# Optimization experiments

Hardware: AMD Instinct MI355X
Metric: run time of the kernel (lower is better)

The kernel has to match this reference:

```python
import math
import jax, jax.numpy as jnp
import numpy as np

DIM = 1024
N_HEADS = 16
HEAD_DIM = DIM // N_HEADS
SEQ_LEN = 2048
BASE = 10000.0
EPS = 1e-5


def rope_cache(seq_len, dim):
    pos = jnp.arange(seq_len, dtype=jnp.float32)[:, None]          # (S,1)
    di = jnp.arange(0, dim, 2, dtype=jnp.float32) / dim            # (d/2,)
    theta = pos * jnp.exp(-di * math.log(BASE))                    # (S,d/2)
    cos = jnp.repeat(jnp.cos(theta), 2, axis=1)                    # (S,d)
    sin = jnp.repeat(jnp.sin(theta), 2, axis=1)
    return cos, sin


def rotate_half(x):
    # NOTE: faithful to source: concatenate (-odd, even), not interleave
    x1 = x[..., ::2]
    x2 = x[..., 1::2]
    return jnp.concatenate((-x2, x1), axis=-1)


def layernorm(x, gamma, beta):
    mu = jnp.mean(x, axis=-1, keepdims=True)
    var = jnp.var(x, axis=-1, keepdims=True)
    return (x - mu) * jax.lax.rsqrt(var + EPS) * gamma + beta


def setup_inputs() -> dict:
    key = jax.random.key(0)
    ks = jax.random.split(key, 7)
    s = 1.0 / math.sqrt(DIM)
    return {
        "x": jax.random.normal(ks[0], (2, SEQ_LEN, DIM), dtype=jnp.float32),
        "Wq": jax.random.normal(ks[1], (DIM, DIM), dtype=jnp.float32) * s,
        "Wk": jax.random.normal(ks[2], (DIM, DIM), dtype=jnp.float32) * s,
        "Wv": jax.random.normal(ks[3], (DIM, DIM), dtype=jnp.float32) * s,
        "q_gamma": jnp.ones((HEAD_DIM,), jnp.float32),
        "q_beta": jnp.zeros((HEAD_DIM,), jnp.float32),
        "k_gamma": jnp.ones((HEAD_DIM,), jnp.float32),
        "k_beta": jnp.zeros((HEAD_DIM,), jnp.float32),
        "Wo": jax.random.normal(ks[4], (DIM, DIM), dtype=jnp.float32) * s,
        "bo": jnp.zeros((DIM,), jnp.float32),
    }


def reference(x, Wq, Wk, Wv, q_gamma, q_beta, k_gamma, k_beta, Wo, bo):
    B, S, D = x.shape
    H, hd = N_HEADS, HEAD_DIM
    # QKV projections (torch Linear: x @ W.T)
    q = (x @ Wq.T).reshape(B, S, H, hd).transpose(0, 2, 1, 3)  # (B,H,S,hd)
    k = (x @ Wk.T).reshape(B, S, H, hd).transpose(0, 2, 1, 3)
    v = (x @ Wv.T).reshape(B, S, H, hd).transpose(0, 2, 1, 3)
    # QK-norm over head_dim
    q = layernorm(q, q_gamma, q_beta)
    k = layernorm(k, k_gamma, k_beta)
    # RoPE
    cos, sin = rope_cache(S, hd)  # (S,hd)
    cos = cos[None, None]
    sin = sin[None, None]
    q = q * cos + rotate_half(q) * sin
    k = k * cos + rotate_half(k) * sin
    # causal attention
    scale = 1.0 / math.sqrt(hd)
    scores = scale * jnp.einsum('bhqd,bhkd->bhqk', q, k)
    mask = jnp.tril(jnp.ones((S, S), dtype=bool))
    scores = jnp.where(mask, scores, -jnp.inf)
    attn = jax.nn.softmax(scores, axis=-1)
    out = jnp.einsum('bhqk,bhkd->bhqd', attn, v)
    out = out.transpose(0, 2, 1, 3).reshape(B, S, D)
    return out @ Wo.T + bo
```

## Files before the change

### kernel.cpp

```cpp
#include <hip/hip_runtime.h>
#include <hip/hip_bf16.h>

#define SEQ   2048
#define NH    16
#define HD    64
#define BATCH 2
#define DIMM  1024

typedef __attribute__((ext_vector_type(8))) __bf16 bfrag;
typedef __attribute__((ext_vector_type(4))) float f32x4;

__device__ __forceinline__ short f2b(float f) {
  unsigned x = __float_as_uint(f);
  x += 0x7fff + ((x >> 16) & 1);
  return (short)(x >> 16);
}
__device__ __forceinline__ float b2f(short s) {
  unsigned u = ((unsigned)(unsigned short)s) << 16;
  return __uint_as_float(u);
}
__device__ __forceinline__ short f2b_pk(float f) {
  unsigned r;
  asm("v_cvt_pk_bf16_f32 %0, %1, %1" : "=v"(r) : "v"(f));
  return (short)r;
}

__device__ __forceinline__ void gload16(const void* g, void* l) {
  __builtin_amdgcn_global_load_lds(
      (const __attribute__((address_space(1))) void*)g,
      (__attribute__((address_space(3))) void*)l, 16, 0, 0);
}

__global__ __launch_bounds__(256) void k_prep(
    const float* __restrict__ x, const float* __restrict__ w0,
    const float* __restrict__ w1, const float* __restrict__ w2,
    const float* __restrict__ w3, short* __restrict__ xb,
    short* __restrict__ wb, float* __restrict__ cstab) {
  int b = blockIdx.x;
  if (b < 4096) {
    int i = b * 256 + threadIdx.x;
    float4 v = reinterpret_cast<const float4*>(x)[i];
    short4 o;
    o.x = f2b(v.x); o.y = f2b(v.y); o.z = f2b(v.z); o.w = f2b(v.w);
    reinterpret_cast<short4*>(xb)[i] = o;
  } else if (b < 8192) {
    int bb = b - 4096;
    int widx = bb >> 10;
    const float* src = widx == 0 ? w0 : (widx == 1 ? w1 : (widx == 2 ? w2 : w3));
    int i = (bb & 1023) * 256 + threadIdx.x;
    float4 v = reinterpret_cast<const float4*>(src)[i];
    short4 o;
    o.x = f2b(v.x); o.y = f2b(v.y); o.z = f2b(v.z); o.w = f2b(v.w);
    reinterpret_cast<short4*>(wb + (size_t)widx * 1048576)[i] = o;
  } else {
    int gid = (b - 8192) * 256 + threadIdx.x;
    int s = gid >> 5, i = gid & 31;
    float freq = expf(-(float)(2 * i) * (1.0f / 64.0f) * 9.210340371976184f);
    float th = (float)s * freq;
    cstab[gid * 2]     = cosf(th);
    cstab[gid * 2 + 1] = sinf(th);
  }
}

__global__ __launch_bounds__(256) void k_gemm_qkv(
    const short* __restrict__ xb, const short* __restrict__ wb,
    short* __restrict__ Qh, short* __restrict__ Kh, short* __restrict__ Vt) {
  __shared__ alignas(16) short As[2][128 * 64];
  __shared__ alignas(16) short Bs[2][128 * 64];
  const int tid = threadIdx.x;
  const int lane = tid & 63, w = tid >> 6;
  const int wr = w >> 1, wc = w & 1;
  const int id = blockIdx.x;
  const int xcd = id & 7, j = id >> 3;
  const int bn = xcd * 3 + j % 3;
  const int bm = j / 3;
  const int widx = bn >> 3;
  const int brow0 = (bn & 7) * 128;
  const short* Wp = wb + (size_t)widx * (1 << 20);

  const int l15 = lane & 15, lq = lane >> 4, l7 = lane & 7;
  const int srow = lane >> 3;
  const int sslot = l7 ^ srow;

  f32x4 acc[4][4] = {};

  auto STAGE = [&](int buf, int kk) {
#pragma unroll
    for (int p = 0; p < 4; ++p) {
      int rr = p * 32 + w * 8 + srow;
      gload16(&xb[(size_t)(bm * 128 + rr) * 1024 + kk + sslot * 8],
              &As[buf][p * 2048 + w * 512]);
      gload16(&Wp[(size_t)(brow0 + rr) * 1024 + kk + sslot * 8],
              &Bs[buf][p * 2048 + w * 512]);
    }
  };

  STAGE(0, 0);
  __syncthreads();
  int cur = 0;
#pragma unroll 1
  for (int t = 0; t < 16; ++t) {
    if (t + 1 < 16) STAGE(cur ^ 1, (t + 1) * 64);
#pragma unroll
    for (int ks = 0; ks < 2; ++ks) {
      bfrag af[4], bf[4];
      int slot = (ks * 4 + lq) ^ l7;
#pragma unroll
      for (int mi = 0; mi < 4; ++mi)
        af[mi] = *(const bfrag*)&As[cur][(wr * 64 + mi * 16 + l15) * 64 + slot * 8];
#pragma unroll
      for (int ni = 0; ni < 4; ++ni)
        bf[ni] = *(const bfrag*)&Bs[cur][(wc * 64 + ni * 16 + l15) * 64 + slot * 8];
      __builtin_amdgcn_s_setprio(1);
#pragma unroll
      for (int mi = 0; mi < 4; ++mi)
#pragma unroll
        for (int ni = 0; ni < 4; ++ni)
          acc[mi][ni] = __builtin_amdgcn_mfma_f32_16x16x32_bf16(af[mi], bf[ni], acc[mi][ni], 0, 0, 0);
      __builtin_amdgcn_s_setprio(0);
    }
    __syncthreads();
    cur ^= 1;
  }

  if (widx < 2) {
    short* dst = widx == 0 ? Qh : Kh;
#pragma unroll
    for (int mi = 0; mi < 4; ++mi) {
#pragma unroll
      for (int ni = 0; ni < 4; ++ni) {
        int ng = bn * 128 + wc * 64 + ni * 16 + l15;
        int col = ng & 1023, h = col >> 6, d = col & 63;
#pragma unroll
        for (int r = 0; r < 4; ++r) {
          int mg = bm * 128 + wr * 64 + mi * 16 + lq * 4 + r;
          int b = mg >> 11, s = mg & 2047;
          dst[((size_t)((b * 16 + h) * 2048 + s)) * 64 + d] = f2b(acc[mi][ni][r]);
        }
      }
    }
  } else {
#pragma unroll
    for (int mi = 0; mi < 4; ++mi) {
#pragma unroll
      for (int ni = 0; ni < 4; ++ni) {
        int ng = bn * 128 + wc * 64 + ni * 16 + l15;
        int col = ng & 1023, h = col >> 6, d = col & 63;
        int mg0 = bm * 128 + wr * 64 + mi * 16 + lq * 4;
        int b = mg0 >> 11, s0 = mg0 & 2047;
        short4 sv;
        sv.x = f2b(acc[mi][ni][0]); sv.y = f2b(acc[mi][ni][1]);
        sv.z = f2b(acc[mi][ni][2]); sv.w = f2b(acc[mi][ni][3]);
        *reinterpret_cast<short4*>(
            &Vt[((size_t)((b * 16 + h) * 64 + d)) * 2048 + s0]) = sv;
      }
    }
  }
}

__global__ __launch_bounds__(256) void k_ln_rope(
    short* __restrict__ Qh, short* __restrict__ Kh,
    const float* __restrict__ qg, const float* __restrict__ qb_,
    const float* __restrict__ kg, const float* __restrict__ kb_,
    const float* __restrict__ cstab) {
  __shared__ float Ysh[32 * 64];
  const int tid = threadIdx.x;
  const int rloc = tid >> 3;
  const int g = tid & 7;
  const int d0 = g * 8;
  const int row = blockIdx.x * 32 + rloc;
  const int which = blockIdx.y;
  short* ptr = which ? Kh : Qh;
  const float* gamma = which ? kg : qg;
  const float* beta  = which ? kb_ : qb_;
  const int s = row & 2047;

  short vs[8];
  *reinterpret_cast<uint4*>(vs) =
      *reinterpret_cast<const uint4*>(&ptr[(size_t)row * 64 + d0]);
  float x[8];
#pragma unroll
  for (int j = 0; j < 8; ++j) x[j] = b2f(vs[j]);
  float s1 = 0.0f, s2 = 0.0f;
#pragma unroll
  for (int j = 0; j < 8; ++j) { s1 += x[j]; s2 = fmaf(x[j], x[j], s2); }
#pragma unroll
  for (int off = 1; off < 8; off <<= 1) {
    s1 += __shfl_xor(s1, off, 8);
    s2 += __shfl_xor(s2, off, 8);
  }
  float mu = s1 * (1.0f / 64.0f);
  float var = s2 * (1.0f / 64.0f) - mu * mu;
  float rs = rsqrtf(var + 1e-5f);

  float gv[8], bv[8];
  *reinterpret_cast<float4*>(&gv[0]) = *reinterpret_cast<const float4*>(&gamma[d0]);
  *reinterpret_cast<float4*>(&gv[4]) = *reinterpret_cast<const float4*>(&gamma[d0 + 4]);
  *reinterpret_cast<float4*>(&bv[0]) = *reinterpret_cast<const float4*>(&beta[d0]);
  *reinterpret_cast<float4*>(&bv[4]) = *reinterpret_cast<const float4*>(&beta[d0 + 4]);
  float y[8];
#pragma unroll
  for (int j = 0; j < 8; ++j) y[j] = (x[j] - mu) * rs * gv[j] + bv[j];

  *reinterpret_cast<float4*>(&Ysh[rloc * 64 + d0])     = *reinterpret_cast<float4*>(&y[0]);
  *reinterpret_cast<float4*>(&Ysh[rloc * 64 + d0 + 4]) = *reinterpret_cast<float4*>(&y[4]);
  __syncthreads();

  float2 cs4[4];
  *reinterpret_cast<float4*>(&cs4[0]) =
      *reinterpret_cast<const float4*>(&cstab[((size_t)s * 32 + g * 4) * 2]);
  *reinterpret_cast<float4*>(&cs4[2]) =
      *reinterpret_cast<const float4*>(&cstab[((size_t)s * 32 + g * 4 + 2) * 2]);

  short o[8];
#pragma unroll
  for (int j = 0; j < 8; ++j) {
    int d = d0 + j;
    float pv = (d < 32) ? Ysh[rloc * 64 + 2 * d + 1]
                        : Ysh[rloc * 64 + 2 * (d - 32)];
    float c = cs4[j >> 1].x, sn = cs4[j >> 1].y;
    float ov = (d < 32) ? (y[j] * c - pv * sn) : (y[j] * c + pv * sn);
    o[j] = f2b_pk(ov);
  }
  *reinterpret_cast<uint4*>(&ptr[(size_t)row * 64 + d0]) =
      *reinterpret_cast<uint4*>(o);
}

__global__ __launch_bounds__(256) void k_attn(
    const short* __restrict__ Qh, const short* __restrict__ Kh,
    const short* __restrict__ Vtg, short* __restrict__ Ob) {
  __shared__ alignas(16) short Ks[2][64 * 64];
  __shared__ alignas(16) short Vs[2][64 * 64];
  __shared__ alignas(16) short Ps[4][16 * 64];
  const int id = blockIdx.x;
  const int xcd = id & 7;
  const int idx = id >> 3;
  const int qt = 31 - (idx >> 2);
  const int bh = xcd * 4 + (idx & 3);
  const int b = bh >> 4, h = bh & 15;
  const int tid = threadIdx.x, lane = tid & 63, w = tid >> 6;
  const short* Qp = Qh + (size_t)bh * SEQ * 64;
  const short* Kp = Kh + (size_t)bh * SEQ * 64;
  const short* Vp = Vtg + (size_t)bh * 64 * SEQ;

  const int srow = lane >> 3;
  const int sslot = (lane & 7) ^ srow;

  const int l15 = lane & 15;
  const int l7 = lane & 7;
  const int lq = lane >> 4;

  auto STAGE = [&](int buf, int kb) {
#pragma unroll
    for (int j = 0; j < 2; ++j) {
      int rr = w * 16 + j * 8 + srow;
      gload16(&Kp[(size_t)(kb * 64 + rr) * 64 + sslot * 8],
              &Ks[buf][w * 1024 + j * 512]);
      gload16(&Vp[(size_t)rr * 2048 + kb * 64 + sslot * 8],
              &Vs[buf][w * 1024 + j * 512]);
    }
  };

  const int nkb = qt + 1;

  const int qrow_l = qt * 64 + w * 16 + l15;
  bfrag qf[2];
#pragma unroll
  for (int c = 0; c < 2; ++c)
    qf[c] = *(const bfrag*)&Qp[(size_t)qrow_l * 64 + c * 32 + lq * 8];

  f32x4 oacc[4] = {};
  float lrow[4] = {0.0f, 0.0f, 0.0f, 0.0f};

  auto body = [&](int kb, int cur, bool diag) {
    f32x4 sacc[4] = {};
    __builtin_amdgcn_s_setprio(1);
#pragma unroll
    for (int c2 = 0; c2 < 4; ++c2) {
      int krow = c2 * 16 + l15;
#pragma unroll
      for (int dc = 0; dc < 2; ++dc) {
        int slot = (dc * 4 + lq) ^ l7;
        bfrag kf = *(const bfrag*)&Ks[cur][krow * 64 + slot * 8];
        sacc[c2] = __builtin_amdgcn_mfma_f32_16x16x32_bf16(qf[dc], kf, sacc[c2], 0, 0, 0);
      }
    }
    __builtin_amdgcn_s_setprio(0);

    const int qg0 = qt * 64 + w * 16 + lq * 4;
#pragma unroll
    for (int r = 0; r < 4; ++r) {
      float pv4[4];
#pragma unroll
      for (int c2 = 0; c2 < 4; ++c2) {
        float s2 = fmaf(sacc[c2][r], 0.18033688011112042f, -11.541560327111707f);
        if (diag && (kb * 64 + c2 * 16 + l15 > qg0 + r)) s2 = -1e30f;
        pv4[c2] = __builtin_amdgcn_exp2f(s2);
      }
      lrow[r] += (pv4[0] + pv4[1]) + (pv4[2] + pv4[3]);
      int row = lq * 4 + r;
#pragma unroll
      for (int c2 = 0; c2 < 4; ++c2) {
        int swz = (c2 * 2 + (l15 >> 3)) ^ (row & 7);
        Ps[w][row * 64 + swz * 8 + (l15 & 7)] = f2b_pk(pv4[c2]);
      }
    }

    bfrag pf[2];
#pragma unroll
    for (int kf2 = 0; kf2 < 2; ++kf2)
      pf[kf2] = *(const bfrag*)&Ps[w][l15 * 64 + (((kf2 * 4 + lq) ^ l7) * 8)];
    __builtin_amdgcn_s_setprio(1);
#pragma unroll
    for (int dc = 0; dc < 4; ++dc) {
      int drow = dc * 16 + l15;
#pragma unroll
      for (int kf2 = 0; kf2 < 2; ++kf2) {
        int slot = (kf2 * 4 + lq) ^ l7;
        bfrag vf = *(const bfrag*)&Vs[cur][drow * 64 + slot * 8];
        oacc[dc] = __builtin_amdgcn_mfma_f32_16x16x32_bf16(pf[kf2], vf, oacc[dc], 0, 0, 0);
      }
    }
    __builtin_amdgcn_s_setprio(0);
  };

  STAGE(0, 0);
  __syncthreads();

  int cur = 0;
#pragma unroll 1
  for (int kb = 0; kb < nkb - 1; ++kb) {
    STAGE(cur ^ 1, kb + 1);
    body(kb, cur, false);
    __syncthreads();
    cur ^= 1;
  }
  body(nkb - 1, cur, true);

  float inv[4];
#pragma unroll
  for (int r = 0; r < 4; ++r) {
#pragma unroll
    for (int off = 1; off < 16; off <<= 1) lrow[r] += __shfl_xor(lrow[r], off);
    inv[r] = 1.0f / lrow[r];
  }
#pragma unroll
  for (int dc = 0; dc < 4; ++dc) {
#pragma unroll
    for (int r = 0; r < 4; ++r) {
      int qg = qt * 64 + w * 16 + lq * 4 + r;
      Ob[(size_t)(b * SEQ + qg) * 1024 + h * 64 + dc * 16 + l15] =
          f2b(oacc[dc][r] * inv[r]);
    }
  }
}

__global__ __launch_bounds__(256) void k_gemm_out(
    const short* __restrict__ Ab, const short* __restrict__ Wp,
    const float* __restrict__ bo, float* __restrict__ out) {
  __shared__ alignas(16) short As[2][64 * 64];
  __shared__ alignas(16) short Bs[2][128 * 64];
  const int tid = threadIdx.x;
  const int lane = tid & 63, w = tid >> 6;
  const int id = blockIdx.x;
  const int bn = id & 7, bm = id >> 3;
  const int brow0 = bn * 128;

  const int l15 = lane & 15, lq = lane >> 4, l7 = lane & 7;
  const int srow = lane >> 3;
  const int sslot = l7 ^ srow;

  f32x4 acc[4][2] = {};

  auto STAGE = [&](int buf, int kk) {
#pragma unroll
    for (int p = 0; p < 2; ++p) {
      int rr = p * 32 + w * 8 + srow;
      gload16(&Ab[(size_t)(bm * 64 + rr) * 1024 + kk + sslot * 8],
              &As[buf][p * 2048 + w * 512]);
    }
#pragma unroll
    for (int p = 0; p < 4; ++p) {
      int rr = p * 32 + w * 8 + srow;
      gload16(&Wp[(size_t)(brow0 + rr) * 1024 + kk + sslot * 8],
              &Bs[buf][p * 2048 + w * 512]);
    }
  };

  STAGE(0, 0);
  __syncthreads();
  int cur = 0;
#pragma unroll 1
  for (int t = 0; t < 16; ++t) {
    if (t + 1 < 16) STAGE(cur ^ 1, (t + 1) * 64);
#pragma unroll
    for (int ks = 0; ks < 2; ++ks) {
      bfrag af[4], bf[2];
      int slot = (ks * 4 + lq) ^ l7;
#pragma unroll
      for (int mi = 0; mi < 4; ++mi)
        af[mi] = *(const bfrag*)&As[cur][(mi * 16 + l15) * 64 + slot * 8];
#pragma unroll
      for (int ni = 0; ni < 2; ++ni)
        bf[ni] = *(const bfrag*)&Bs[cur][(w * 32 + ni * 16 + l15) * 64 + slot * 8];
      __builtin_amdgcn_s_setprio(1);
#pragma unroll
      for (int mi = 0; mi < 4; ++mi)
#pragma unroll
        for (int ni = 0; ni < 2; ++ni)
          acc[mi][ni] = __builtin_amdgcn_mfma_f32_16x16x32_bf16(af[mi], bf[ni], acc[mi][ni], 0, 0, 0);
      __builtin_amdgcn_s_setprio(0);
    }
    __syncthreads();
    cur ^= 1;
  }

#pragma unroll
  for (int mi = 0; mi < 4; ++mi) {
#pragma unroll
    for (int ni = 0; ni < 2; ++ni) {
      int ng = bn * 128 + w * 32 + ni * 16 + l15;
      float bias = bo[ng];
#pragma unroll
      for (int r = 0; r < 4; ++r) {
        int mg = bm * 64 + mi * 16 + lq * 4 + r;
        out[(size_t)mg * 1024 + ng] = acc[mi][ni][r] + bias;
      }
    }
  }
}

extern "C" void kernel_launch(void* const* d_in, const int* in_sizes, int n_in,
                              void* d_out, int out_size, void* d_ws, size_t ws_size,
                              hipStream_t stream) {
  const float* x  = (const float*)d_in[0];
  const float* Wq = (const float*)d_in[1];
  const float* Wk = (const float*)d_in[2];
  const float* Wv = (const float*)d_in[3];
  const float* qgamma = (const float*)d_in[4];
  const float* qbeta  = (const float*)d_in[5];
  const float* kgamma = (const float*)d_in[6];
  const float* kbeta  = (const float*)d_in[7];
  const float* Wo = (const float*)d_in[8];
  const float* bo = (const float*)d_in[9];
  float* out = (float*)d_out;

  char* ws = (char*)d_ws;
  short* xb    = (short*)(ws);
  short* wb    = (short*)(ws + 8388608);
  short* Qh    = (short*)(ws + 16777216);
  short* Kh    = (short*)(ws + 25165824);
  short* Vt    = (short*)(ws + 33554432);
  short* Obuf  = (short*)(ws + 41943040);
  float* cstab = (float*)(ws + 50331648);

  k_prep<<<8448, 256, 0, stream>>>(x, Wq, Wk, Wv, Wo, xb, wb, cstab);

  k_gemm_qkv<<<768, 256, 0, stream>>>(xb, wb, Qh, Kh, Vt);
  k_ln_rope<<<dim3(2048, 2), 256, 0, stream>>>(
      Qh, Kh, qgamma, qbeta, kgamma, kbeta, cstab);
  k_attn<<<1024, 256, 0, stream>>>(Qh, Kh, Vt, Obuf);
  k_gemm_out<<<512, 256, 0, stream>>>(Obuf, wb + 3145728, bo, out);
}
```

Measured before the change: 117.8 us.

## Transpose QK^T MFMA to pass P to PV via register shuffles, drop LDS staging

Swaps the MFMA operand order for the score computation so each lane holds scores for one query row across four keys. The probabilities are then packed to bf16 pairs and redistributed with cross-lane shuffles into the A-fragment layout for the PV MFMA, which removes the per-wave shared-memory P buffer and its write/read round trip. Row sums become a single accumulator reduced across lane groups at the end. In exchange it adds 16 shuffles (ds_bpermute) plus selects per block, which may cost about as much as the LDS traffic it replaces.

After: 120.6 us. 1.02x slower.

```diff
diff --git a/kernel.cpp b/kernel.cpp
--- a/kernel.cpp
+++ b/kernel.cpp
@@ -23,6 +23,11 @@
   unsigned r;
   asm("v_cvt_pk_bf16_f32 %0, %1, %1" : "=v"(r) : "v"(f));
   return (short)r;
+}
+__device__ __forceinline__ unsigned cvtpk2(float lo, float hi) {
+  unsigned r;
+  asm("v_cvt_pk_bf16_f32 %0, %1, %2" : "=v"(r) : "v"(lo), "v"(hi));
+  return r;
 }
 
 __device__ __forceinline__ void gload16(const void* g, void* l) {
@@ -231,7 +236,6 @@
     const short* __restrict__ Vtg, short* __restrict__ Ob) {
   __shared__ alignas(16) short Ks[2][64 * 64];
   __shared__ alignas(16) short Vs[2][64 * 64];
-  __shared__ alignas(16) short Ps[4][16 * 64];
   const int id = blockIdx.x;
   const int xcd = id & 7;
   const int idx = id >> 3;
@@ -270,7 +274,11 @@
     qf[c] = *(const bfrag*)&Qp[(size_t)qrow_l * 64 + c * 32 + lq * 8];
 
   f32x4 oacc[4] = {};
-  float lrow[4] = {0.0f, 0.0f, 0.0f, 0.0f};
+  float lrow = 0.0f;
+
+  const int src_a = l15 + (((2 * lq) & 3) << 4);
+  const int src_b = l15 + (((2 * lq + 1) & 3) << 4);
+  const bool hisel = (lq >> 1) != 0;
 
   auto body = [&](int kb, int cur, bool diag) {
     f32x4 sacc[4] = {};
@@ -282,34 +290,50 @@
       for (int dc = 0; dc < 2; ++dc) {
         int slot = (dc * 4 + lq) ^ l7;
         bfrag kf = *(const bfrag*)&Ks[cur][krow * 64 + slot * 8];
-        sacc[c2] = __builtin_amdgcn_mfma_f32_16x16x32_bf16(qf[dc], kf, sacc[c2], 0, 0, 0);
+        sacc[c2] = __builtin_amdgcn_mfma_f32_16x16x32_bf16(kf, qf[dc], sacc[c2], 0, 0, 0);
       }
     }
     __builtin_amdgcn_s_setprio(0);
 
-    const int qg0 = qt * 64 + w * 16 + lq * 4;
-#pragma unroll
-    for (int r = 0; r < 4; ++r) {
-      float pv4[4];
-#pragma unroll
-      for (int c2 = 0; c2 < 4; ++c2) {
+    const int qg = qt * 64 + w * 16 + l15;
+    float p[4][4];
+#pragma unroll
+    for (int c2 = 0; c2 < 4; ++c2) {
+      int k0 = kb * 64 + c2 * 16 + lq * 4;
+#pragma unroll
+      for (int r = 0; r < 4; ++r) {
         float s2 = fmaf(sacc[c2][r], 0.18033688011112042f, -11.541560327111707f);
-        if (diag && (kb * 64 + c2 * 16 + l15 > qg0 + r)) s2 = -1e30f;
-        pv4[c2] = __builtin_amdgcn_exp2f(s2);
-      }
-      lrow[r] += (pv4[0] + pv4[1]) + (pv4[2] + pv4[3]);
-      int row = lq * 4 + r;
-#pragma unroll
-      for (int c2 = 0; c2 < 4; ++c2) {
-        int swz = (c2 * 2 + (l15 >> 3)) ^ (row & 7);
-        Ps[w][row * 64 + swz * 8 + (l15 & 7)] = f2b_pk(pv4[c2]);
-      }
-    }
-
+        if (diag && (k0 + r > qg)) s2 = -1e30f;
+        p[c2][r] = __builtin_amdgcn_exp2f(s2);
+      }
+      lrow += (p[c2][0] + p[c2][1]) + (p[c2][2] + p[c2][3]);
+    }
+
+    unsigned pk[4][2];
+#pragma unroll
+    for (int c2 = 0; c2 < 4; ++c2) {
+      pk[c2][0] = cvtpk2(p[c2][0], p[c2][1]);
+      pk[c2][1] = cvtpk2(p[c2][2], p[c2][3]);
+    }
     bfrag pf[2];
 #pragma unroll
-    for (int kf2 = 0; kf2 < 2; ++kf2)
-      pf[kf2] = *(const bfrag*)&Ps[w][l15 * 64 + (((kf2 * 4 + lq) ^ l7) * 8)];
+    for (int kf2 = 0; kf2 < 2; ++kf2) {
+      unsigned u[4];
+#pragma unroll
+      for (int bhalf = 0; bhalf < 2; ++bhalf) {
+        int src = bhalf ? src_b : src_a;
+        unsigned lo0 = __shfl(pk[2 * kf2][0], src);
+        unsigned lo1 = __shfl(pk[2 * kf2][1], src);
+        unsigned hi0 = __shfl(pk[2 * kf2 + 1][0], src);
+        unsigned hi1 = __shfl(pk[2 * kf2 + 1][1], src);
+        u[bhalf * 2 + 0] = hisel ? hi0 : lo0;
+        u[bhalf * 2 + 1] = hisel ? hi1 : lo1;
+      }
+      union { bfrag f; unsigned v[4]; } uu;
+      uu.v[0] = u[0]; uu.v[1] = u[1]; uu.v[2] = u[2]; uu.v[3] = u[3];
+      pf[kf2] = uu.f;
+    }
+
     __builtin_amdgcn_s_setprio(1);
 #pragma unroll
     for (int dc = 0; dc < 4; ++dc) {
@@ -337,13 +361,12 @@
   }
   body(nkb - 1, cur, true);
 
+  lrow += __shfl_xor(lrow, 16);
+  lrow += __shfl_xor(lrow, 32);
   float inv[4];
 #pragma unroll
-  for (int r = 0; r < 4; ++r) {
-#pragma unroll
-    for (int off = 1; off < 16; off <<= 1) lrow[r] += __shfl_xor(lrow[r], off);
-    inv[r] = 1.0f / lrow[r];
-  }
+  for (int r = 0; r < 4; ++r)
+    inv[r] = 1.0f / __shfl(lrow, lq * 4 + r);
 #pragma unroll
   for (int dc = 0; dc < 4; ++dc) {
 #pragma unroll
```
